# Kernel tuning notes

Hardware: AMD Instinct MI355X
Metric: run time of the kernel (lower is better)

Reference implementation:

```python
import jax, jax.numpy as jnp
import numpy as np
from math import sqrt

NQ, NV = 4096, 4096
QIN = KIN = VIN = 1024
NHEADS, DK = 8, 512
HEAD_DIM = DK // NHEADS  # 64


def setup_inputs() -> dict:
    key = jax.random.key(0)
    k1, k2, k3, k4, k5, k6 = jax.random.split(key, 6)
    qin = jax.random.normal(k1, (NQ, QIN), dtype=jnp.float32)
    kin = jax.random.normal(k2, (NV, KIN), dtype=jnp.float32)
    vin = jax.random.normal(k3, (NV, VIN), dtype=jnp.float32)
    # Parameters initialized as randn / (head_dim * in_dim), matching the torch module.
    Wqs = jax.random.normal(k4, (NHEADS, HEAD_DIM, QIN), dtype=jnp.float32) / (HEAD_DIM * QIN)
    Wks = jax.random.normal(k5, (NHEADS, HEAD_DIM, KIN), dtype=jnp.float32) / (HEAD_DIM * KIN)
    Wvs = jax.random.normal(k6, (NHEADS, HEAD_DIM, VIN), dtype=jnp.float32) / (HEAD_DIM * VIN)
    return {"qin": qin, "kin": kin, "vin": vin, "Wqs": Wqs, "Wks": Wks, "Wvs": Wvs}


def reference(qin, kin, vin, Wqs, Wks, Wvs):
    # Per-head projections: [h, seq, head_dim]
    Qs = jnp.einsum('qi,hoi->hqo', qin, Wqs)
    Ks = jnp.einsum('ki,hoi->hko', kin, Wks)
    Vs = jnp.einsum('vi,hoi->hvo', vin, Wvs)
    scale = 1.0 / sqrt(HEAD_DIM)  # original divides by sqrt(Q.shape[-1]) = head_dim
    scores = jnp.einsum('hqo,hko->hqk', Qs, Ks) * scale  # [h, nq, nv]
    attn = jax.nn.softmax(scores, axis=-1)
    out = jnp.einsum('hqk,hko->hqo', attn, Vs)           # [h, nq, head_dim]
    # concat over heads along last dim -> [nq, nheads*head_dim]
    return jnp.transpose(out, (1, 0, 2)).reshape(out.shape[1], NHEADS * HEAD_DIM)
```

## Files before the change

kernel.cpp:

```cpp
#include <hip/hip_runtime.h>
#include <hip/hip_bf16.h>

#define NQ 4096
#define NKV 4096
#define DIN 1024
#define NH 8
#define HD 64
#define DMODEL 512
#define NSPLIT 2
#define KVHALF (NKV / NSPLIT)

typedef __attribute__((ext_vector_type(4))) float f32x4;
typedef __attribute__((ext_vector_type(8))) short short8;

#define GPTR(p) ((const __attribute__((address_space(1))) void*)(p))
#define SPTR(p) ((__attribute__((address_space(3))) void*)(p))
#define SWZ(r) ((((r) ^ ((r) >> 3)) & 7) << 3)

#define SM_SCALE 0.1803368801111204f

__device__ __forceinline__ ushort f2b(float f) {
  uint u = __float_as_uint(f);
  u = (u + 0x7fffu + ((u >> 16) & 1u)) >> 16;
  return (ushort)u;
}

__device__ __forceinline__ uint cvt_pk_bf16(float lo, float hi) {
  uint r;
  asm("v_cvt_pk_bf16_f32 %0, %1, %2" : "=v"(r) : "v"(lo), "v"(hi));
  return r;
}

__device__ __forceinline__ float fast_exp2(float x) {
  float r;
  asm("v_exp_f32 %0, %1" : "=v"(r) : "v"(x));
  return r;
}

__global__ void cast3_kernel(const float* __restrict__ s0, const float* __restrict__ s1,
                             const float* __restrict__ s2, ushort* __restrict__ d0,
                             ushort* __restrict__ d1, ushort* __restrict__ d2, int shift) {
  const int n4 = 1 << shift;
  const int total = 3 * n4;
  for (int u = blockIdx.x * blockDim.x + threadIdx.x; u < total;
       u += gridDim.x * blockDim.x) {
    const int a = u >> shift;
    const int off = u & (n4 - 1);
    const float4* src = (const float4*)(a == 0 ? s0 : a == 1 ? s1 : s2);
    ushort* dst = a == 0 ? d0 : a == 1 ? d1 : d2;
    float4 v = src[off];
    ushort4 o = make_ushort4(f2b(v.x), f2b(v.y), f2b(v.z), f2b(v.w));
    ((ushort4*)dst)[off] = o;
  }
}

__global__ __launch_bounds__(256) void proj_gemm(
    const ushort* __restrict__ A0, const ushort* __restrict__ B0, ushort* __restrict__ C0,
    const ushort* __restrict__ A1, const ushort* __restrict__ B1, ushort* __restrict__ C1,
    const ushort* __restrict__ A2, const ushort* __restrict__ B2, ushort* __restrict__ C2) {
  const int z = blockIdx.z;
  const ushort* A = z == 0 ? A0 : z == 1 ? A1 : A2;
  const ushort* B = z == 0 ? B0 : z == 1 ? B1 : B2;
  ushort* C = z == 0 ? C0 : z == 1 ? C1 : C2;

  __shared__ ushort As[64 * 32];
  __shared__ ushort Bs[128 * 32];
  const int tid = threadIdx.x;
  const int w = tid >> 6, lane = tid & 63;
  const int wr = w >> 1, wc = w & 1;
  const int bm = blockIdx.x, bn = blockIdx.y;
  const int l15 = lane & 15, l4 = lane >> 4;

  f32x4 acc[2][4];
#pragma unroll
  for (int m = 0; m < 2; ++m)
#pragma unroll
    for (int n = 0; n < 4; ++n) acc[m][n] = (f32x4){0.f, 0.f, 0.f, 0.f};

  const size_t abase = (size_t)(bm * 64) * DIN;
  const size_t bbase = (size_t)(bn * 128) * DIN;
  const int srow = lane >> 2;
  const int schunk = (lane & 3) * 8;

  const int fcol = l4 * 8;

  for (int k0 = 0; k0 < DIN; k0 += 32) {
    __builtin_amdgcn_global_load_lds(
        GPTR(A + abase + (size_t)(w * 16 + srow) * DIN + k0 + schunk),
        SPTR(As + w * 512), 16, 0, 0);
#pragma unroll
    for (int j = 0; j < 2; ++j) {
      const int slot = w * 2 + j;
      __builtin_amdgcn_global_load_lds(
          GPTR(B + bbase + (size_t)(slot * 16 + srow) * DIN + k0 + schunk),
          SPTR(Bs + slot * 512), 16, 0, 0);
    }
    __syncthreads();
    short8 af[2], bfr[4];
#pragma unroll
    for (int m = 0; m < 2; ++m)
      af[m] = *(const short8*)(As + (wr * 32 + m * 16 + l15) * 32 + fcol);
#pragma unroll
    for (int n = 0; n < 4; ++n)
      bfr[n] = *(const short8*)(Bs + (wc * 64 + n * 16 + l15) * 32 + fcol);
#pragma unroll
    for (int m = 0; m < 2; ++m)
#pragma unroll
      for (int n = 0; n < 4; ++n)
        acc[m][n] = __builtin_amdgcn_mfma_f32_16x16x32_bf16(af[m], bfr[n], acc[m][n], 0, 0, 0);
    __syncthreads();
  }

  const int orow = bm * 64 + wr * 32 + l4 * 4;
  const int ocol = bn * 128 + wc * 64 + l15;
#pragma unroll
  for (int m = 0; m < 2; ++m)
#pragma unroll
    for (int n = 0; n < 4; ++n)
#pragma unroll
      for (int r = 0; r < 4; ++r)
        C[(size_t)(orow + m * 16 + r) * DMODEL + ocol + n * 16] = f2b(acc[m][n][r]);
}

__global__ __launch_bounds__(256) void attn_kernel(
    const ushort* __restrict__ Qp, const ushort* __restrict__ Kp,
    const ushort* __restrict__ Vp, float* __restrict__ Opart,
    float* __restrict__ Mpart, float* __restrict__ Lpart) {
  __shared__ ushort Ks[2][64 * 64];
  __shared__ ushort Vt[2][64 * 64];
  __shared__ ushort Ps[64 * 64];
  const int h = blockIdx.y;
  const int q0 = blockIdx.x * 64;
  const int split = blockIdx.z;
  const int kvbase = split * KVHALF;
  const int tid = threadIdx.x;
  const int w = tid >> 6, lane = tid & 63;
  const int l15 = lane & 15, l4 = lane >> 4;

  const int lrow = lane >> 3, lch = lane & 7;
  int srow[2], sch[2];
#pragma unroll
  for (int j = 0; j < 2; ++j) {
    const int row = (w * 2 + j) * 8 + lrow;
    srow[j] = row;
    sch[j] = (lch ^ ((row ^ (row >> 3)) & 7)) * 8;
  }
  const int vkv = w * 16 + (lane & 7) * 2;
  const int vd0 = ((lane >> 3) & 7) * 8;

#pragma unroll
  for (int j = 0; j < 2; ++j)
    __builtin_amdgcn_global_load_lds(
        GPTR(Qp + (size_t)(q0 + srow[j]) * DMODEL + h * HD + sch[j]),
        SPTR(Ps + (w * 2 + j) * 512), 16, 0, 0);
#pragma unroll
  for (int j = 0; j < 2; ++j)
    __builtin_amdgcn_global_load_lds(
        GPTR(Kp + (size_t)(kvbase + srow[j]) * DMODEL + h * HD + sch[j]),
        SPTR(Ks[0] + (w * 2 + j) * 512), 16, 0, 0);
  short8 vr0 = *(const short8*)(Vp + (size_t)(kvbase + vkv) * DMODEL + h * HD + vd0);
  short8 vr1 = *(const short8*)(Vp + (size_t)(kvbase + vkv + 1) * DMODEL + h * HD + vd0);
  asm volatile("s_waitcnt vmcnt(0)" ::: "memory");
  short8 qa0, qa1;
  {
    const int q = w * 16 + l15;
    const int sw = SWZ(q);
    qa0 = *(const short8*)(Ps + q * 64 + ((8 * l4) ^ sw));
    qa1 = *(const short8*)(Ps + q * 64 + ((32 + 8 * l4) ^ sw));
  }
#pragma unroll
  for (int j = 0; j < 8; ++j) {
    const int d = vd0 + j;
    const uint val = (uint)(ushort)vr0[j] | ((uint)(ushort)vr1[j] << 16);
    *(uint*)(Vt[0] + d * 64 + (vkv ^ SWZ(d))) = val;
  }
  __syncthreads();

  float m_run = -1e30f, l_run = 0.f;
  f32x4 of[4];
#pragma unroll
  for (int fd = 0; fd < 4; ++fd) of[fd] = (f32x4){0.f, 0.f, 0.f, 0.f};

  int cur = 0;
  for (int it = 0; it < KVHALF / 64; ++it) {
    short8 pv0, pv1;
    const bool pf = (it + 1) < KVHALF / 64;
    if (pf) {
      const int kvn = kvbase + (it + 1) * 64;
#pragma unroll
      for (int j = 0; j < 2; ++j)
        __builtin_amdgcn_global_load_lds(
            GPTR(Kp + (size_t)(kvn + srow[j]) * DMODEL + h * HD + sch[j]),
            SPTR(Ks[cur ^ 1] + (w * 2 + j) * 512), 16, 0, 0);
      pv0 = *(const short8*)(Vp + (size_t)(kvn + vkv) * DMODEL + h * HD + vd0);
      pv1 = *(const short8*)(Vp + (size_t)(kvn + vkv + 1) * DMODEL + h * HD + vd0);
    }

    f32x4 sf[4];
#pragma unroll
    for (int fn = 0; fn < 4; ++fn) sf[fn] = (f32x4){0.f, 0.f, 0.f, 0.f};
#pragma unroll
    for (int fn = 0; fn < 4; ++fn) {
      const int kvr = fn * 16 + l15;
      const int sw = SWZ(kvr);
      short8 kb0 = *(const short8*)(Ks[cur] + kvr * 64 + ((8 * l4) ^ sw));
      short8 kb1 = *(const short8*)(Ks[cur] + kvr * 64 + ((32 + 8 * l4) ^ sw));
      sf[fn] = __builtin_amdgcn_mfma_f32_16x16x32_bf16(kb0, qa0, sf[fn], 0, 0, 0);
      sf[fn] = __builtin_amdgcn_mfma_f32_16x16x32_bf16(kb1, qa1, sf[fn], 0, 0, 0);
    }

    float t0 = fmaxf(fmaxf(sf[0][0], sf[0][1]), fmaxf(sf[0][2], sf[0][3]));
    float t1 = fmaxf(fmaxf(sf[1][0], sf[1][1]), fmaxf(sf[1][2], sf[1][3]));
    float t2 = fmaxf(fmaxf(sf[2][0], sf[2][1]), fmaxf(sf[2][2], sf[2][3]));
    float t3 = fmaxf(fmaxf(sf[3][0], sf[3][1]), fmaxf(sf[3][2], sf[3][3]));
    float rmax2 = fmaxf(fmaxf(t0, t1), fmaxf(t2, t3)) * SM_SCALE;
    rmax2 = fmaxf(rmax2, __shfl_xor(rmax2, 16));
    rmax2 = fmaxf(rmax2, __shfl_xor(rmax2, 32));
    if (__any(rmax2 > m_run + 8.0f)) {
      const float mnew = fmaxf(m_run, rmax2);
      const float alpha = fast_exp2(m_run - mnew);
      m_run = mnew;
      l_run *= alpha;
      float ar[4];
#pragma unroll
      for (int r = 0; r < 4; ++r) ar[r] = __shfl(alpha, l4 * 4 + r);
#pragma unroll
      for (int fd = 0; fd < 4; ++fd)
#pragma unroll
        for (int r = 0; r < 4; ++r) of[fd][r] *= ar[r];
    }
    float p[4][4];
    float rsum = 0.f;
#pragma unroll
    for (int fn = 0; fn < 4; ++fn)
#pragma unroll
      for (int r = 0; r < 4; ++r) {
        const float v = fast_exp2(__builtin_fmaf(sf[fn][r], SM_SCALE, -m_run));
        p[fn][r] = v;
        rsum += v;
      }
    rsum += __shfl_xor(rsum, 16);
    rsum += __shfl_xor(rsum, 32);
    l_run += rsum;

    {
      const int q = w * 16 + l15;
      const int sw = SWZ(q);
#pragma unroll
      for (int fn = 0; fn < 4; ++fn) {
        uint2 u;
        u.x = cvt_pk_bf16(p[fn][0], p[fn][1]);
        u.y = cvt_pk_bf16(p[fn][2], p[fn][3]);
        *(uint2*)(Ps + q * 64 + ((fn * 16 + l4 * 4) ^ sw)) = u;
      }
    }
    asm volatile("s_waitcnt lgkmcnt(0)" ::: "memory");
    __builtin_amdgcn_sched_barrier(0);

    {
      const int q = w * 16 + l15;
      const int swp = SWZ(q);
      short8 pa0 = *(const short8*)(Ps + q * 64 + ((8 * l4) ^ swp));
      short8 pa1 = *(const short8*)(Ps + q * 64 + ((32 + 8 * l4) ^ swp));
#pragma unroll
      for (int fd = 0; fd < 4; ++fd) {
        const int dr = fd * 16 + l15;
        const int sw = SWZ(dr);
        short8 vb0 = *(const short8*)(Vt[cur] + dr * 64 + ((8 * l4) ^ sw));
        short8 vb1 = *(const short8*)(Vt[cur] + dr * 64 + ((32 + 8 * l4) ^ sw));
        of[fd] = __builtin_amdgcn_mfma_f32_16x16x32_bf16(pa0, vb0, of[fd], 0, 0, 0);
        of[fd] = __builtin_amdgcn_mfma_f32_16x16x32_bf16(pa1, vb1, of[fd], 0, 0, 0);
      }
    }

    if (pf) {
#pragma unroll
      for (int j = 0; j < 8; ++j) {
        const int d = vd0 + j;
        const uint val = (uint)(ushort)pv0[j] | ((uint)(ushort)pv1[j] << 16);
        *(uint*)(Vt[cur ^ 1] + d * 64 + (vkv ^ SWZ(d))) = val;
      }
    }
    __syncthreads();
    cur ^= 1;
  }

#pragma unroll
  for (int r = 0; r < 4; ++r) {
    const int qrow = q0 + w * 16 + l4 * 4 + r;
#pragma unroll
    for (int fd = 0; fd < 4; ++fd)
      Opart[(size_t)split * (NQ * DMODEL) + (size_t)qrow * DMODEL + h * HD + fd * 16 + l15] =
          of[fd][r];
  }
  if (l4 == 0) {
    const int qrow = q0 + w * 16 + l15;
    Mpart[(split * NH + h) * NQ + qrow] = m_run;
    Lpart[(split * NH + h) * NQ + qrow] = l_run;
  }
}

__global__ __launch_bounds__(256) void merge_kernel(
    const float* __restrict__ Opart, const float* __restrict__ Mpart,
    const float* __restrict__ Lpart, float* __restrict__ out) {
  const int i4 = blockIdx.x * 256 + threadIdx.x;
  const int i = i4 * 4;
  const int q = i >> 9;
  const int col = i & 511;
  const int h = col >> 6;
  const float m0 = Mpart[h * NQ + q];
  const float m1 = Mpart[NH * NQ + h * NQ + q];
  const float mm = fmaxf(m0, m1);
  const float w0 = fast_exp2(m0 - mm);
  const float w1 = fast_exp2(m1 - mm);
  const float l = w0 * Lpart[h * NQ + q] + w1 * Lpart[NH * NQ + h * NQ + q];
  const float inv = 1.0f / l;
  const float4 o0 = ((const float4*)Opart)[i4];
  const float4 o1 = ((const float4*)(Opart + (size_t)NQ * DMODEL))[i4];
  float4 o;
  o.x = (w0 * o0.x + w1 * o1.x) * inv;
  o.y = (w0 * o0.y + w1 * o1.y) * inv;
  o.z = (w0 * o0.z + w1 * o1.z) * inv;
  o.w = (w0 * o0.w + w1 * o1.w) * inv;
  ((float4*)out)[i4] = o;
}

extern "C" void kernel_launch(void* const* d_in, const int* in_sizes, int n_in,
                              void* d_out, int out_size, void* d_ws, size_t ws_size,
                              hipStream_t stream) {
  const float* qin = (const float*)d_in[0];
  const float* kin = (const float*)d_in[1];
  const float* vin = (const float*)d_in[2];
  const float* Wq = (const float*)d_in[3];
  const float* Wk = (const float*)d_in[4];
  const float* Wv = (const float*)d_in[5];
  float* out = (float*)d_out;

  char* ws = (char*)d_ws;
  size_t off = 0;
  ushort* qb = (ushort*)(ws + off); off += (size_t)NQ * DIN * 2;
  ushort* kb = (ushort*)(ws + off); off += (size_t)NKV * DIN * 2;
  ushort* vb = (ushort*)(ws + off); off += (size_t)NKV * DIN * 2;
  ushort* wqb = (ushort*)(ws + off); off += (size_t)DMODEL * DIN * 2;
  ushort* wkb = (ushort*)(ws + off); off += (size_t)DMODEL * DIN * 2;
  ushort* wvb = (ushort*)(ws + off); off += (size_t)DMODEL * DIN * 2;
  ushort* Qp = (ushort*)(ws + off); off += (size_t)NQ * DMODEL * 2;
  ushort* Kp = (ushort*)(ws + off); off += (size_t)NKV * DMODEL * 2;
  ushort* Vp = (ushort*)(ws + off); off += (size_t)NKV * DMODEL * 2;
  float* Opart = (float*)(ws + off); off += (size_t)NSPLIT * NQ * DMODEL * 4;
  float* Mpart = (float*)(ws + off); off += (size_t)NSPLIT * NH * NQ * 4;
  float* Lpart = (float*)(ws + off); off += (size_t)NSPLIT * NH * NQ * 4;

  cast3_kernel<<<2048, 256, 0, stream>>>(qin, kin, vin, qb, kb, vb, 20);
  cast3_kernel<<<1536, 256, 0, stream>>>(Wq, Wk, Wv, wqb, wkb, wvb, 17);
  proj_gemm<<<dim3(64, 4, 3), 256, 0, stream>>>(qb, wqb, Qp, kb, wkb, Kp, vb, wvb, Vp);
  attn_kernel<<<dim3(64, NH, NSPLIT), 256, 0, stream>>>(Qp, Kp, Vp, Opart, Mpart, Lpart);
  merge_kernel<<<(NQ * DMODEL / 4) / 256, 256, 0, stream>>>(Opart, Mpart, Lpart, out);
}
```

Before: 226.4 us.

## Double query rows per attention block, split KV four ways, reuse workspace

```diff
diff --git a/kernel.cpp b/kernel.cpp
--- a/kernel.cpp
+++ b/kernel.cpp
@@ -7,8 +7,9 @@
 #define NH 8
 #define HD 64
 #define DMODEL 512
-#define NSPLIT 2
-#define KVHALF (NKV / NSPLIT)
+#define NSPLIT 4
+#define KVQ (NKV / NSPLIT)
+#define QBLK 128
 
 typedef __attribute__((ext_vector_type(4))) float f32x4;
 typedef __attribute__((ext_vector_type(8))) short short8;
@@ -35,6 +36,40 @@
   float r;
   asm("v_exp_f32 %0, %1" : "=v"(r) : "v"(x));
   return r;
+}
+
+__device__ __forceinline__ float red_max4(float x) {
+  float a, b;
+  asm("v_mov_b32 %0, %2\n\t"
+      "v_mov_b32 %1, %2\n\t"
+      "v_permlane32_swap_b32 %0, %1"
+      : "=&v"(a), "=&v"(b)
+      : "v"(x));
+  const float m1 = fmaxf(a, b);
+  float c, d;
+  asm("v_mov_b32 %0, %2\n\t"
+      "v_mov_b32 %1, %2\n\t"
+      "v_permlane16_swap_b32 %0, %1"
+      : "=&v"(c), "=&v"(d)
+      : "v"(m1));
+  return fmaxf(c, d);
+}
+
+__device__ __forceinline__ float red_sum4(float x) {
+  float a, b;
+  asm("v_mov_b32 %0, %2\n\t"
+      "v_mov_b32 %1, %2\n\t"
+      "v_permlane32_swap_b32 %0, %1"
+      : "=&v"(a), "=&v"(b)
+      : "v"(x));
+  const float s = a + b;
+  float c, d;
+  asm("v_mov_b32 %0, %2\n\t"
+      "v_mov_b32 %1, %2\n\t"
+      "v_permlane16_swap_b32 %0, %1"
+      : "=&v"(c), "=&v"(d)
+      : "v"(s));
+  return c + d;
 }
 
 __global__ void cast3_kernel(const float* __restrict__ s0, const float* __restrict__ s1,
@@ -81,7 +116,6 @@
   const size_t bbase = (size_t)(bn * 128) * DIN;
   const int srow = lane >> 2;
   const int schunk = (lane & 3) * 8;
-
   const int fcol = l4 * 8;
 
   for (int k0 = 0; k0 < DIN; k0 += 32) {
@@ -122,17 +156,17 @@
         C[(size_t)(orow + m * 16 + r) * DMODEL + ocol + n * 16] = f2b(acc[m][n][r]);
 }
 
-__global__ __launch_bounds__(256) void attn_kernel(
+__global__ __launch_bounds__(256, 3) void attn_kernel(
     const ushort* __restrict__ Qp, const ushort* __restrict__ Kp,
     const ushort* __restrict__ Vp, float* __restrict__ Opart,
     float* __restrict__ Mpart, float* __restrict__ Lpart) {
   __shared__ ushort Ks[2][64 * 64];
   __shared__ ushort Vt[2][64 * 64];
-  __shared__ ushort Ps[64 * 64];
+  __shared__ ushort Ps[QBLK * 64];
   const int h = blockIdx.y;
-  const int q0 = blockIdx.x * 64;
+  const int q0 = blockIdx.x * QBLK;
   const int split = blockIdx.z;
-  const int kvbase = split * KVHALF;
+  const int kvbase = split * KVQ;
   const int tid = threadIdx.x;
   const int w = tid >> 6, lane = tid & 63;
   const int l15 = lane & 15, l4 = lane >> 4;
@@ -149,10 +183,13 @@
   const int vd0 = ((lane >> 3) & 7) * 8;
 
 #pragma unroll
-  for (int j = 0; j < 2; ++j)
+  for (int j = 0; j < 4; ++j) {
+    const int row = (w * 4 + j) * 8 + lrow;
+    const int ch = (lch ^ ((row ^ (row >> 3)) & 7)) * 8;
     __builtin_amdgcn_global_load_lds(
-        GPTR(Qp + (size_t)(q0 + srow[j]) * DMODEL + h * HD + sch[j]),
-        SPTR(Ps + (w * 2 + j) * 512), 16, 0, 0);
+        GPTR(Qp + (size_t)(q0 + row) * DMODEL + h * HD + ch),
+        SPTR(Ps + (w * 4 + j) * 512), 16, 0, 0);
+  }
 #pragma unroll
   for (int j = 0; j < 2; ++j)
     __builtin_amdgcn_global_load_lds(
@@ -161,12 +198,13 @@
   short8 vr0 = *(const short8*)(Vp + (size_t)(kvbase + vkv) * DMODEL + h * HD + vd0);
   short8 vr1 = *(const short8*)(Vp + (size_t)(kvbase + vkv + 1) * DMODEL + h * HD + vd0);
   asm volatile("s_waitcnt vmcnt(0)" ::: "memory");
-  short8 qa0, qa1;
-  {
-    const int q = w * 16 + l15;
+  short8 qa[2][2];
+#pragma unroll
+  for (int fq = 0; fq < 2; ++fq) {
+    const int q = w * 32 + fq * 16 + l15;
     const int sw = SWZ(q);
-    qa0 = *(const short8*)(Ps + q * 64 + ((8 * l4) ^ sw));
-    qa1 = *(const short8*)(Ps + q * 64 + ((32 + 8 * l4) ^ sw));
+    qa[fq][0] = *(const short8*)(Ps + q * 64 + ((8 * l4) ^ sw));
+    qa[fq][1] = *(const short8*)(Ps + q * 64 + ((32 + 8 * l4) ^ sw));
   }
 #pragma unroll
   for (int j = 0; j < 8; ++j) {
@@ -176,15 +214,17 @@
   }
   __syncthreads();
 
-  float m_run = -1e30f, l_run = 0.f;
-  f32x4 of[4];
-#pragma unroll
-  for (int fd = 0; fd < 4; ++fd) of[fd] = (f32x4){0.f, 0.f, 0.f, 0.f};
+  float m_run[2] = {-1e30f, -1e30f}, l_run[2] = {0.f, 0.f};
+  f32x4 of[2][4];
+#pragma unroll
+  for (int fq = 0; fq < 2; ++fq)
+#pragma unroll
+    for (int fd = 0; fd < 4; ++fd) of[fq][fd] = (f32x4){0.f, 0.f, 0.f, 0.f};
 
   int cur = 0;
-  for (int it = 0; it < KVHALF / 64; ++it) {
+  for (int it = 0; it < KVQ / 64; ++it) {
     short8 pv0, pv1;
-    const bool pf = (it + 1) < KVHALF / 64;
+    const bool pf = (it + 1) < KVQ / 64;
     if (pf) {
       const int kvn = kvbase + (it + 1) * 64;
 #pragma unroll
@@ -196,61 +236,64 @@
       pv1 = *(const short8*)(Vp + (size_t)(kvn + vkv + 1) * DMODEL + h * HD + vd0);
     }
 
-    f32x4 sf[4];
-#pragma unroll
-    for (int fn = 0; fn < 4; ++fn) sf[fn] = (f32x4){0.f, 0.f, 0.f, 0.f};
+    f32x4 sf[2][4];
+#pragma unroll
+    for (int fq = 0; fq < 2; ++fq)
+#pragma unroll
+      for (int fn = 0; fn < 4; ++fn) sf[fq][fn] = (f32x4){0.f, 0.f, 0.f, 0.f};
 #pragma unroll
     for (int fn = 0; fn < 4; ++fn) {
       const int kvr = fn * 16 + l15;
       const int sw = SWZ(kvr);
       short8 kb0 = *(const short8*)(Ks[cur] + kvr * 64 + ((8 * l4) ^ sw));
       short8 kb1 = *(const short8*)(Ks[cur] + kvr * 64 + ((32 + 8 * l4) ^ sw));
-      sf[fn] = __builtin_amdgcn_mfma_f32_16x16x32_bf16(kb0, qa0, sf[fn], 0, 0, 0);
-      sf[fn] = __builtin_amdgcn_mfma_f32_16x16x32_bf16(kb1, qa1, sf[fn], 0, 0, 0);
-    }
-
-    float t0 = fmaxf(fmaxf(sf[0][0], sf[0][1]), fmaxf(sf[0][2], sf[0][3]));
-    float t1 = fmaxf(fmaxf(sf[1][0], sf[1][1]), fmaxf(sf[1][2], sf[1][3]));
-    float t2 = fmaxf(fmaxf(sf[2][0], sf[2][1]), fmaxf(sf[2][2], sf[2][3]));
-    float t3 = fmaxf(fmaxf(sf[3][0], sf[3][1]), fmaxf(sf[3][2], sf[3][3]));
-    float rmax2 = fmaxf(fmaxf(t0, t1), fmaxf(t2, t3)) * SM_SCALE;
-    rmax2 = fmaxf(rmax2, __shfl_xor(rmax2, 16));
-    rmax2 = fmaxf(rmax2, __shfl_xor(rmax2, 32));
-    if (__any(rmax2 > m_run + 8.0f)) {
-      const float mnew = fmaxf(m_run, rmax2);
-      const float alpha = fast_exp2(m_run - mnew);
-      m_run = mnew;
-      l_run *= alpha;
-      float ar[4];
-#pragma unroll
-      for (int r = 0; r < 4; ++r) ar[r] = __shfl(alpha, l4 * 4 + r);
-#pragma unroll
-      for (int fd = 0; fd < 4; ++fd)
-#pragma unroll
-        for (int r = 0; r < 4; ++r) of[fd][r] *= ar[r];
-    }
-    float p[4][4];
-    float rsum = 0.f;
-#pragma unroll
-    for (int fn = 0; fn < 4; ++fn)
-#pragma unroll
-      for (int r = 0; r < 4; ++r) {
-        const float v = fast_exp2(__builtin_fmaf(sf[fn][r], SM_SCALE, -m_run));
-        p[fn][r] = v;
-        rsum += v;
+      sf[0][fn] = __builtin_amdgcn_mfma_f32_16x16x32_bf16(kb0, qa[0][0], sf[0][fn], 0, 0, 0);
+      sf[0][fn] = __builtin_amdgcn_mfma_f32_16x16x32_bf16(kb1, qa[0][1], sf[0][fn], 0, 0, 0);
+      sf[1][fn] = __builtin_amdgcn_mfma_f32_16x16x32_bf16(kb0, qa[1][0], sf[1][fn], 0, 0, 0);
+      sf[1][fn] = __builtin_amdgcn_mfma_f32_16x16x32_bf16(kb1, qa[1][1], sf[1][fn], 0, 0, 0);
+    }
+
+#pragma unroll
+    for (int fq = 0; fq < 2; ++fq) {
+      float t0 = fmaxf(fmaxf(sf[fq][0][0], sf[fq][0][1]), fmaxf(sf[fq][0][2], sf[fq][0][3]));
+      float t1 = fmaxf(fmaxf(sf[fq][1][0], sf[fq][1][1]), fmaxf(sf[fq][1][2], sf[fq][1][3]));
+      float t2 = fmaxf(fmaxf(sf[fq][2][0], sf[fq][2][1]), fmaxf(sf[fq][2][2], sf[fq][2][3]));
+      float t3 = fmaxf(fmaxf(sf[fq][3][0], sf[fq][3][1]), fmaxf(sf[fq][3][2], sf[fq][3][3]));
+      float rmax2 = red_max4(fmaxf(fmaxf(t0, t1), fmaxf(t2, t3)) * SM_SCALE);
+      if (__any(rmax2 > m_run[fq] + 8.0f)) {
+        const float mnew = fmaxf(m_run[fq], rmax2);
+        const float alpha = fast_exp2(m_run[fq] - mnew);
+        m_run[fq] = mnew;
+        l_run[fq] *= alpha;
+        float ar[4];
+#pragma unroll
+        for (int r = 0; r < 4; ++r) ar[r] = __shfl(alpha, l4 * 4 + r);
+#pragma unroll
+        for (int fd = 0; fd < 4; ++fd)
+#pragma unroll
+          for (int r = 0; r < 4; ++r) of[fq][fd][r] *= ar[r];
       }
-    rsum += __shfl_xor(rsum, 16);
-    rsum += __shfl_xor(rsum, 32);
-    l_run += rsum;
-
-    {
-      const int q = w * 16 + l15;
+      float rsum = 0.f;
+#pragma unroll
+      for (int fn = 0; fn < 4; ++fn)
+#pragma unroll
+        for (int r = 0; r < 4; ++r) {
+          const float v = fast_exp2(__builtin_fmaf(sf[fq][fn][r], SM_SCALE, -m_run[fq]));
+          sf[fq][fn][r] = v;
+          rsum += v;
+        }
+      l_run[fq] += red_sum4(rsum);
+    }
+
+#pragma unroll
+    for (int fq = 0; fq < 2; ++fq) {
+      const int q = w * 32 + fq * 16 + l15;
       const int sw = SWZ(q);
 #pragma unroll
       for (int fn = 0; fn < 4; ++fn) {
         uint2 u;
-        u.x = cvt_pk_bf16(p[fn][0], p[fn][1]);
-        u.y = cvt_pk_bf16(p[fn][2], p[fn][3]);
+        u.x = cvt_pk_bf16(sf[fq][fn][0], sf[fq][fn][1]);
+        u.y = cvt_pk_bf16(sf[fq][fn][2], sf[fq][fn][3]);
         *(uint2*)(Ps + q * 64 + ((fn * 16 + l4 * 4) ^ sw)) = u;
       }
     }
@@ -258,18 +301,24 @@
     __builtin_amdgcn_sched_barrier(0);
 
     {
-      const int q = w * 16 + l15;
-      const int swp = SWZ(q);
-      short8 pa0 = *(const short8*)(Ps + q * 64 + ((8 * l4) ^ swp));
-      short8 pa1 = *(const short8*)(Ps + q * 64 + ((32 + 8 * l4) ^ swp));
+      short8 pa[2][2];
+#pragma unroll
+      for (int fq = 0; fq < 2; ++fq) {
+        const int q = w * 32 + fq * 16 + l15;
+        const int swp = SWZ(q);
+        pa[fq][0] = *(const short8*)(Ps + q * 64 + ((8 * l4) ^ swp));
+        pa[fq][1] = *(const short8*)(Ps + q * 64 + ((32 + 8 * l4) ^ swp));
+      }
 #pragma unroll
       for (int fd = 0; fd < 4; ++fd) {
         const int dr = fd * 16 + l15;
         const int sw = SWZ(dr);
         short8 vb0 = *(const short8*)(Vt[cur] + dr * 64 + ((8 * l4) ^ sw));
         short8 vb1 = *(const short8*)(Vt[cur] + dr * 64 + ((32 + 8 * l4) ^ sw));
-        of[fd] = __builtin_amdgcn_mfma_f32_16x16x32_bf16(pa0, vb0, of[fd], 0, 0, 0);
-        of[fd] = __builtin_amdgcn_mfma_f32_16x16x32_bf16(pa1, vb1, of[fd], 0, 0, 0);
+        of[0][fd] = __builtin_amdgcn_mfma_f32_16x16x32_bf16(pa[0][0], vb0, of[0][fd], 0, 0, 0);
+        of[0][fd] = __builtin_amdgcn_mfma_f32_16x16x32_bf16(pa[0][1], vb1, of[0][fd], 0, 0, 0);
+        of[1][fd] = __builtin_amdgcn_mfma_f32_16x16x32_bf16(pa[1][0], vb0, of[1][fd], 0, 0, 0);
+        of[1][fd] = __builtin_amdgcn_mfma_f32_16x16x32_bf16(pa[1][1], vb1, of[1][fd], 0, 0, 0);
       }
     }
 
@@ -286,17 +335,20 @@
   }
 
 #pragma unroll
-  for (int r = 0; r < 4; ++r) {
-    const int qrow = q0 + w * 16 + l4 * 4 + r;
-#pragma unroll
-    for (int fd = 0; fd < 4; ++fd)
-      Opart[(size_t)split * (NQ * DMODEL) + (size_t)qrow * DMODEL + h * HD + fd * 16 + l15] =
-          of[fd][r];
-  }
-  if (l4 == 0) {
-    const int qrow = q0 + w * 16 + l15;
-    Mpart[(split * NH + h) * NQ + qrow] = m_run;
-    Lpart[(split * NH + h) * NQ + qrow] = l_run;
+  for (int fq = 0; fq < 2; ++fq) {
+#pragma unroll
+    for (int r = 0; r < 4; ++r) {
+      const int qrow = q0 + w * 32 + fq * 16 + l4 * 4 + r;
+#pragma unroll
+      for (int fd = 0; fd < 4; ++fd)
+        Opart[(size_t)split * (NQ * DMODEL) + (size_t)qrow * DMODEL + h * HD + fd * 16 + l15] =
+            of[fq][fd][r];
+    }
+    if (l4 == 0) {
+      const int qrow = q0 + w * 32 + fq * 16 + l15;
+      Mpart[(split * NH + h) * NQ + qrow] = m_run[fq];
+      Lpart[(split * NH + h) * NQ + qrow] = l_run[fq];
+    }
   }
 }
 
@@ -308,20 +360,30 @@
   const int q = i >> 9;
   const int col = i & 511;
   const int h = col >> 6;
-  const float m0 = Mpart[h * NQ + q];
-  const float m1 = Mpart[NH * NQ + h * NQ + q];
-  const float mm = fmaxf(m0, m1);
-  const float w0 = fast_exp2(m0 - mm);
-  const float w1 = fast_exp2(m1 - mm);
-  const float l = w0 * Lpart[h * NQ + q] + w1 * Lpart[NH * NQ + h * NQ + q];
+  float m[NSPLIT];
+  float mm = -1e30f;
+#pragma unroll
+  for (int s = 0; s < NSPLIT; ++s) {
+    m[s] = Mpart[(s * NH + h) * NQ + q];
+    mm = fmaxf(mm, m[s]);
+  }
+  float l = 0.f, ws[NSPLIT];
+#pragma unroll
+  for (int s = 0; s < NSPLIT; ++s) {
+    ws[s] = fast_exp2(m[s] - mm);
+    l += ws[s] * Lpart[(s * NH + h) * NQ + q];
+  }
   const float inv = 1.0f / l;
-  const float4 o0 = ((const float4*)Opart)[i4];
-  const float4 o1 = ((const float4*)(Opart + (size_t)NQ * DMODEL))[i4];
-  float4 o;
-  o.x = (w0 * o0.x + w1 * o1.x) * inv;
-  o.y = (w0 * o0.y + w1 * o1.y) * inv;
-  o.z = (w0 * o0.z + w1 * o1.z) * inv;
-  o.w = (w0 * o0.w + w1 * o1.w) * inv;
+  float4 o = {0.f, 0.f, 0.f, 0.f};
+#pragma unroll
+  for (int s = 0; s < NSPLIT; ++s) {
+    const float4 os = ((const float4*)(Opart + (size_t)s * NQ * DMODEL))[i4];
+    o.x += ws[s] * os.x;
+    o.y += ws[s] * os.y;
+    o.z += ws[s] * os.z;
+    o.w += ws[s] * os.w;
+  }
+  o.x *= inv; o.y *= inv; o.z *= inv; o.w *= inv;
   ((float4*)out)[i4] = o;
 }
 
@@ -337,23 +399,23 @@
   float* out = (float*)d_out;
 
   char* ws = (char*)d_ws;
-  size_t off = 0;
-  ushort* qb = (ushort*)(ws + off); off += (size_t)NQ * DIN * 2;
-  ushort* kb = (ushort*)(ws + off); off += (size_t)NKV * DIN * 2;
-  ushort* vb = (ushort*)(ws + off); off += (size_t)NKV * DIN * 2;
-  ushort* wqb = (ushort*)(ws + off); off += (size_t)DMODEL * DIN * 2;
-  ushort* wkb = (ushort*)(ws + off); off += (size_t)DMODEL * DIN * 2;
-  ushort* wvb = (ushort*)(ws + off); off += (size_t)DMODEL * DIN * 2;
-  ushort* Qp = (ushort*)(ws + off); off += (size_t)NQ * DMODEL * 2;
-  ushort* Kp = (ushort*)(ws + off); off += (size_t)NKV * DMODEL * 2;
-  ushort* Vp = (ushort*)(ws + off); off += (size_t)NKV * DMODEL * 2;
-  float* Opart = (float*)(ws + off); off += (size_t)NSPLIT * NQ * DMODEL * 4;
-  float* Mpart = (float*)(ws + off); off += (size_t)NSPLIT * NH * NQ * 4;
-  float* Lpart = (float*)(ws + off); off += (size_t)NSPLIT * NH * NQ * 4;
+  const size_t MB = 1 << 20;
+  ushort* Qp = (ushort*)(ws + 0 * MB);
+  ushort* Kp = (ushort*)(ws + 4 * MB);
+  ushort* Vp = (ushort*)(ws + 8 * MB);
+  ushort* qb = (ushort*)(ws + 12 * MB);
+  ushort* kb = (ushort*)(ws + 20 * MB);
+  ushort* vb = (ushort*)(ws + 28 * MB);
+  ushort* wqb = (ushort*)(ws + 36 * MB);
+  ushort* wkb = (ushort*)(ws + 37 * MB);
+  ushort* wvb = (ushort*)(ws + 38 * MB);
+  float* Opart = (float*)(ws + 12 * MB);
+  float* Mpart = (float*)(ws + 44 * MB);
+  float* Lpart = (float*)(ws + 44 * MB + 512 * 1024);
 
   cast3_kernel<<<2048, 256, 0, stream>>>(qin, kin, vin, qb, kb, vb, 20);
   cast3_kernel<<<1536, 256, 0, stream>>>(Wq, Wk, Wv, wqb, wkb, wvb, 17);
   proj_gemm<<<dim3(64, 4, 3), 256, 0, stream>>>(qb, wqb, Qp, kb, wkb, Kp, vb, wvb, Vp);
-  attn_kernel<<<dim3(64, NH, NSPLIT), 256, 0, stream>>>(Qp, Kp, Vp, Opart, Mpart, Lpart);
+  attn_kernel<<<dim3(NQ / QBLK, NH, NSPLIT), 256, 0, stream>>>(Qp, Kp, Vp, Opart, Mpart, Lpart);
   merge_kernel<<<(NQ * DMODEL / 4) / 256, 256, 0, stream>>>(Opart, Mpart, Lpart, out);
 }
```

New measurement: 198.1 us. 1.14x faster.
